# Optimization experiments

Measured on AMD Instinct MI355X. Metric: run time of the kernel, lower is better.

The kernel has to match this reference:

```python
import jax, jax.numpy as jnp
import numpy as np

N_NODES = 100000
HIDDEN = 128
N_EDGES = 1600000


def setup_inputs() -> dict:
    key = jax.random.key(0)
    k_z, k_e, k_w1, k_b1, k_w2, k_b2 = jax.random.split(key, 6)
    z = jax.random.normal(k_z, (N_NODES, HIDDEN), dtype=jnp.float32)
    edge_index = jax.random.randint(k_e, (2, N_EDGES), 0, N_NODES, dtype=jnp.int64)
    # torch.nn.Linear default init: U(-1/sqrt(fan_in), 1/sqrt(fan_in))
    lim1 = 1.0 / np.sqrt(2 * HIDDEN)
    W1 = jax.random.uniform(k_w1, (2 * HIDDEN, HIDDEN), minval=-lim1, maxval=lim1, dtype=jnp.float32)
    b1 = jax.random.uniform(k_b1, (HIDDEN,), minval=-lim1, maxval=lim1, dtype=jnp.float32)
    lim2 = 1.0 / np.sqrt(HIDDEN)
    W2 = jax.random.uniform(k_w2, (HIDDEN, 1), minval=-lim2, maxval=lim2, dtype=jnp.float32)
    b2 = jax.random.uniform(k_b2, (1,), minval=-lim2, maxval=lim2, dtype=jnp.float32)
    return {"z": z, "edge_index": edge_index, "W1": W1, "b1": b1, "W2": W2, "b2": b2}


def reference(z, edge_index, W1, b1, W2, b2):
    src = edge_index[0]
    dst = edge_index[1]
    # gather node pairs -> concat: [E, 2H]
    edge_feat = jnp.concatenate([z[src], z[dst]], axis=1)
    h = jax.nn.relu(edge_feat @ W1 + b1)  # [E, H]
    score = h @ W2 + b2                   # [E, 1]
    return score
```

## Files before the change

### kernel.cpp

```cpp
#include <hip/hip_runtime.h>
#include <hip/hip_bf16.h>
#include <stdint.h>

#define HIDDEN 128
#define EPG 8
#define NBLK_SORT 256
#define NBUK 256

typedef __attribute__((ext_vector_type(8))) short bf16x8;
typedef __attribute__((ext_vector_type(16))) float f32x16;

static __device__ __forceinline__ uint32_t cvt2(float a, float b) {
    union { __hip_bfloat162 h2; uint32_t u; } c;
    c.h2 = __float22bfloat162_rn(make_float2(a, b));
    return c.u;
}
static __device__ __forceinline__ float bf_lo(uint32_t p) {
    union { uint32_t u; float f; } v; v.u = p << 16; return v.f;
}
static __device__ __forceinline__ float bf_hi(uint32_t p) {
    union { uint32_t u; float f; } v; v.u = p & 0xffff0000u; return v.f;
}

__global__ __launch_bounds__(256) void transpose_w1(
    const float* __restrict__ W1, unsigned short* __restrict__ Wt)
{
    const int t = blockIdx.x * 256 + threadIdx.x;
    if (t >= 4096) return;
    const int cc = t >> 4;
    const int kg = t & 15;
    const int ccol = cc & 127;
    const int kofs = (cc >= 128) ? 128 : 0;
    uint32_t u[4];
    #pragma unroll
    for (int p = 0; p < 4; ++p) {
        const float a = W1[(size_t)(kofs + kg * 8 + 2 * p) * 128 + ccol];
        const float b = W1[(size_t)(kofs + kg * 8 + 2 * p + 1) * 128 + ccol];
        u[p] = cvt2(a, b);
    }
    uint4 o = { u[0], u[1], u[2], u[3] };
    *reinterpret_cast<uint4*>(Wt + (size_t)cc * 128 + kg * 8) = o;
}

__global__ __launch_bounds__(256) void precompute_mfma32(
    const float* __restrict__ z, const float* __restrict__ W1,
    const unsigned short* __restrict__ Wt,
    unsigned short* __restrict__ UV, int n_nodes, int n_groups)
{
    __shared__ char Zt[32 * 256];
    __shared__ char Sm[32 * 512];

    const int tid = threadIdx.x;
    const int lane = tid & 63;
    const int w = tid >> 6;
    const int nl = lane & 31;
    const int hi = lane >> 5;

    const int st_node = tid >> 3;
    const int st_j2 = tid & 7;
    const int st_swz = (st_node & 7) << 4;
    const int st_addrA = st_node * 256 + ((st_j2 * 32) ^ st_swz);
    const int st_addrB = st_node * 256 + ((st_j2 * 32 + 16) ^ st_swz);

    bf16x8 wf[2][8];
    if (Wt) {
        #pragma unroll
        for (int cg = 0; cg < 2; ++cg) {
            const int cc = w * 64 + cg * 32 + nl;
            #pragma unroll
            for (int ks = 0; ks < 8; ++ks)
                wf[cg][ks] = *reinterpret_cast<const bf16x8*>(
                    Wt + (size_t)cc * 128 + ks * 16 + hi * 8);
        }
    } else {
        #pragma unroll
        for (int cg = 0; cg < 2; ++cg) {
            const int cc = w * 64 + cg * 32 + nl;
            const int ccol = cc & 127;
            const int kofs = (cc >= 128) ? 128 : 0;
            #pragma unroll
            for (int ks = 0; ks < 8; ++ks) {
                const int k0 = ks * 16 + hi * 8 + kofs;
                float t[8];
                #pragma unroll
                for (int j = 0; j < 8; ++j)
                    t[j] = W1[(size_t)(k0 + j) * 128 + ccol];
                union { uint32_t u[4]; bf16x8 v; } fu;
                fu.u[0] = cvt2(t[0], t[1]); fu.u[1] = cvt2(t[2], t[3]);
                fu.u[2] = cvt2(t[4], t[5]); fu.u[3] = cvt2(t[6], t[7]);
                wf[cg][ks] = fu.v;
            }
        }
    }

    const int stride = gridDim.x;
    int ng = blockIdx.x;
    if (ng >= n_groups) return;

    float4 nz0, nz1, nz2, nz3;
    {
        int node = ng * 32 + st_node;
        node = (node < n_nodes) ? node : (n_nodes - 1);
        const float* zp = z + (size_t)node * HIDDEN + st_j2 * 16;
        nz0 = *reinterpret_cast<const float4*>(zp);
        nz1 = *reinterpret_cast<const float4*>(zp + 4);
        nz2 = *reinterpret_cast<const float4*>(zp + 8);
        nz3 = *reinterpret_cast<const float4*>(zp + 12);
    }

    while (ng < n_groups) {
        {
            uint4 A, B;
            A.x = cvt2(nz0.x, nz0.y); A.y = cvt2(nz0.z, nz0.w);
            A.z = cvt2(nz1.x, nz1.y); A.w = cvt2(nz1.z, nz1.w);
            B.x = cvt2(nz2.x, nz2.y); B.y = cvt2(nz2.z, nz2.w);
            B.z = cvt2(nz3.x, nz3.y); B.w = cvt2(nz3.z, nz3.w);
            *reinterpret_cast<uint4*>(Zt + st_addrA) = A;
            *reinterpret_cast<uint4*>(Zt + st_addrB) = B;
        }

        const int ngn = ng + stride;
        if (ngn < n_groups) {
            int node = ngn * 32 + st_node;
            node = (node < n_nodes) ? node : (n_nodes - 1);
            const float* zp = z + (size_t)node * HIDDEN + st_j2 * 16;
            nz0 = *reinterpret_cast<const float4*>(zp);
            nz1 = *reinterpret_cast<const float4*>(zp + 4);
            nz2 = *reinterpret_cast<const float4*>(zp + 8);
            nz3 = *reinterpret_cast<const float4*>(zp + 12);
        }

        __syncthreads();

        {
            const int rd_swz = (nl & 7) << 4;
            bf16x8 zf[8];
            #pragma unroll
            for (int ks = 0; ks < 8; ++ks) {
                const int off = ks * 32 + hi * 16;
                zf[ks] = *reinterpret_cast<const bf16x8*>(
                    Zt + nl * 256 + (off ^ rd_swz));
            }

            f32x16 acc0 = {};
            f32x16 acc1 = {};
            #pragma unroll
            for (int ks = 0; ks < 8; ++ks) {
                acc0 = __builtin_amdgcn_mfma_f32_32x32x16_bf16(wf[0][ks], zf[ks], acc0, 0, 0, 0);
                acc1 = __builtin_amdgcn_mfma_f32_32x32x16_bf16(wf[1][ks], zf[ks], acc1, 0, 0, 0);
            }

            const int swz = (nl & 15) << 3;
            #pragma unroll
            for (int g = 0; g < 4; ++g) {
                uint2 s0, s1;
                s0.x = cvt2(acc0[4 * g + 0], acc0[4 * g + 1]);
                s0.y = cvt2(acc0[4 * g + 2], acc0[4 * g + 3]);
                s1.x = cvt2(acc1[4 * g + 0], acc1[4 * g + 1]);
                s1.y = cvt2(acc1[4 * g + 2], acc1[4 * g + 3]);
                const int colb0 = w * 128 + g * 16 + hi * 8;
                const int colb1 = w * 128 + 64 + g * 16 + hi * 8;
                *reinterpret_cast<uint2*>(Sm + nl * 512 + (colb0 ^ swz)) = s0;
                *reinterpret_cast<uint2*>(Sm + nl * 512 + (colb1 ^ swz)) = s1;
            }
        }

        __syncthreads();

        {
            const int colb0 = (tid & 31) * 16;
            #pragma unroll
            for (int rep = 0; rep < 4; ++rep) {
                const int node_local = rep * 8 + (tid >> 5);
                const int swz = (node_local & 15) << 3;
                const uint2 g0 = *reinterpret_cast<const uint2*>(Sm + node_local * 512 + ((colb0) ^ swz));
                const uint2 g1 = *reinterpret_cast<const uint2*>(Sm + node_local * 512 + ((colb0 + 8) ^ swz));
                const int node = ng * 32 + node_local;
                if (node < n_nodes) {
                    uint4 o = { g0.x, g0.y, g1.x, g1.y };
                    *reinterpret_cast<uint4*>(UV + (size_t)node * 256 + (tid & 31) * 8) = o;
                }
            }
        }

        ng = ngn;
    }
}

__global__ __launch_bounds__(256) void hist2(
    const int* __restrict__ ei, int* __restrict__ h,
    int n_edges, int chunk, int sh)
{
    __shared__ int lh[NBUK];
    const int t = threadIdx.x;
    if (t < NBUK) lh[t] = 0;
    __syncthreads();
    const int e0 = blockIdx.x * chunk;
    const int e1 = min(e0 + chunk, n_edges);
    for (int e = e0 + t; e < e1; e += 256)
        atomicAdd(&lh[((unsigned)ei[e]) >> sh], 1);
    __syncthreads();
    if (t < NBUK) h[t * NBLK_SORT + blockIdx.x] = lh[t];
}

__global__ __launch_bounds__(NBLK_SORT) void scanP1(
    int* __restrict__ h, int* __restrict__ rowtot)
{
    __shared__ int s[NBLK_SORT];
    const int b = blockIdx.x, t = threadIdx.x;
    const int v = h[b * NBLK_SORT + t];
    s[t] = v;
    __syncthreads();
    for (int d = 1; d < NBLK_SORT; d <<= 1) {
        const int x = (t >= d) ? s[t - d] : 0;
        __syncthreads();
        s[t] += x;
        __syncthreads();
    }
    h[b * NBLK_SORT + t] = s[t] - v;
    if (t == NBLK_SORT - 1) rowtot[b] = s[t];
}

__global__ __launch_bounds__(NBUK) void scanP2(int* __restrict__ rowtot)
{
    __shared__ int s[NBUK];
    const int t = threadIdx.x;
    const int v = rowtot[t];
    s[t] = v;
    __syncthreads();
    for (int d = 1; d < NBUK; d <<= 1) {
        const int x = (t >= d) ? s[t - d] : 0;
        __syncthreads();
        s[t] += x;
        __syncthreads();
    }
    rowtot[t] = s[t] - v;
}

__global__ __launch_bounds__(256) void scatter2(
    const int* __restrict__ ei, const int* __restrict__ h,
    const int* __restrict__ base,
    int2* __restrict__ sd, int* __restrict__ org,
    int n_edges, int chunk, int sh)
{
    __shared__ int lbase[NBUK];
    __shared__ int lrank[NBUK];
    const int t = threadIdx.x;
    if (t < NBUK) {
        lbase[t] = h[t * NBLK_SORT + blockIdx.x] + base[t];
        lrank[t] = 0;
    }
    __syncthreads();
    const int e0 = blockIdx.x * chunk;
    const int e1 = min(e0 + chunk, n_edges);
    for (int e = e0 + t; e < e1; e += 256) {
        const int s = ei[e];
        const int d = ei[n_edges + e];
        const int b = ((unsigned)s) >> sh;
        const int r = atomicAdd(&lrank[b], 1);
        const int pos = lbase[b] + r;
        sd[pos] = make_int2(s, d);
        org[pos] = e;
    }
}

static __device__ __forceinline__ float dot8(uint4 u, uint4 v,
                                             const float* w, const float* bb) {
    const uint32_t up[4] = { u.x, u.y, u.z, u.w };
    const uint32_t vp[4] = { v.x, v.y, v.z, v.w };
    float s = 0.f;
    #pragma unroll
    for (int p = 0; p < 4; ++p) {
        const float h0 = bf_lo(up[p]) + bf_lo(vp[p]) + bb[2 * p];
        const float h1 = bf_hi(up[p]) + bf_hi(vp[p]) + bb[2 * p + 1];
        s = fmaf(fmaxf(h0, 0.f), w[2 * p], s);
        s = fmaf(fmaxf(h1, 0.f), w[2 * p + 1], s);
    }
    return s;
}
static __device__ __forceinline__ float red16(float s) {
    s += __shfl_xor(s, 1, 64); s += __shfl_xor(s, 2, 64);
    s += __shfl_xor(s, 4, 64); s += __shfl_xor(s, 8, 64);
    return s;
}

template <int PACKED>
__global__ __launch_bounds__(256, 4) void edge_score_t(
    const int2* __restrict__ sd, const int* __restrict__ org,
    const int* __restrict__ srcp, const int* __restrict__ dstp,
    const unsigned short* __restrict__ UV,
    const float* __restrict__ b1, const float* __restrict__ W2,
    const float* __restrict__ b2, float* __restrict__ outp, int n_edges)
{
    int vb = blockIdx.x;
    if (PACKED) {
        const int nb = gridDim.x;
        const int q8 = nb >> 3, r8 = nb & 7;
        const int x = blockIdx.x & 7, i = blockIdx.x >> 3;
        vb = (x < r8 ? x * (q8 + 1) : r8 * (q8 + 1) + (x - r8) * q8) + i;
    }

    const int g = (vb * 256 + (int)threadIdx.x) >> 4;
    const int q = threadIdx.x & 15;
    const int e0 = g * EPG;
    if (e0 >= n_edges) return;

    const float4 w2a = *reinterpret_cast<const float4*>(W2 + q * 8);
    const float4 w2b = *reinterpret_cast<const float4*>(W2 + q * 8 + 4);
    const float wloc[8] = { w2a.x, w2a.y, w2a.z, w2a.w, w2b.x, w2b.y, w2b.z, w2b.w };
    const float4 b1a = *reinterpret_cast<const float4*>(b1 + q * 8);
    const float4 b1b = *reinterpret_cast<const float4*>(b1 + q * 8 + 4);
    const float bb[8] = { b1a.x, b1a.y, b1a.z, b1a.w, b1b.x, b1b.y, b1b.z, b1b.w };
    const float bias = b2[0];

    const char* UVb = (const char*)UV;
    const uint32_t qo = (uint32_t)q * 16u;

    if (e0 + EPG - 1 < n_edges) {
        int sidx[EPG], didx[EPG];
        if (PACKED) {
            const int4 p0 = *reinterpret_cast<const int4*>(sd + e0);
            const int4 p1 = *reinterpret_cast<const int4*>(sd + e0 + 2);
            const int4 p2 = *reinterpret_cast<const int4*>(sd + e0 + 4);
            const int4 p3 = *reinterpret_cast<const int4*>(sd + e0 + 6);
            sidx[0]=p0.x; didx[0]=p0.y; sidx[1]=p0.z; didx[1]=p0.w;
            sidx[2]=p1.x; didx[2]=p1.y; sidx[3]=p1.z; didx[3]=p1.w;
            sidx[4]=p2.x; didx[4]=p2.y; sidx[5]=p2.z; didx[5]=p2.w;
            sidx[6]=p3.x; didx[6]=p3.y; sidx[7]=p3.z; didx[7]=p3.w;
        } else {
            const int4 sA = *reinterpret_cast<const int4*>(srcp + e0);
            const int4 sB = *reinterpret_cast<const int4*>(srcp + e0 + 4);
            const int4 dA = *reinterpret_cast<const int4*>(dstp + e0);
            const int4 dB = *reinterpret_cast<const int4*>(dstp + e0 + 4);
            sidx[0]=sA.x; sidx[1]=sA.y; sidx[2]=sA.z; sidx[3]=sA.w;
            sidx[4]=sB.x; sidx[5]=sB.y; sidx[6]=sB.z; sidx[7]=sB.w;
            didx[0]=dA.x; didx[1]=dA.y; didx[2]=dA.z; didx[3]=dA.w;
            didx[4]=dB.x; didx[5]=dB.y; didx[6]=dB.z; didx[7]=dB.w;
        }

        uint4 u[EPG], v[EPG];
        #pragma unroll
        for (int ii = 0; ii < EPG; ++ii) {
            u[ii] = *reinterpret_cast<const uint4*>(UVb + ((uint32_t)sidx[ii] * 512u + qo));
            v[ii] = *reinterpret_cast<const uint4*>(UVb + ((uint32_t)didx[ii] * 512u + 256u + qo));
        }
        __builtin_amdgcn_sched_barrier(0);

        float s[EPG];
        #pragma unroll
        for (int ii = 0; ii < EPG; ++ii) s[ii] = dot8(u[ii], v[ii], wloc, bb);
        #pragma unroll
        for (int ii = 0; ii < EPG; ++ii) s[ii] = red16(s[ii]) + bias;

        if (q == 0) {
            if (PACKED) {
                const int4 o0 = *reinterpret_cast<const int4*>(org + e0);
                const int4 o1 = *reinterpret_cast<const int4*>(org + e0 + 4);
                outp[o0.x] = s[0]; outp[o0.y] = s[1];
                outp[o0.z] = s[2]; outp[o0.w] = s[3];
                outp[o1.x] = s[4]; outp[o1.y] = s[5];
                outp[o1.z] = s[6]; outp[o1.w] = s[7];
            } else {
                float4 oA = { s[0], s[1], s[2], s[3] };
                float4 oB = { s[4], s[5], s[6], s[7] };
                *reinterpret_cast<float4*>(outp + e0) = oA;
                *reinterpret_cast<float4*>(outp + e0 + 4) = oB;
            }
        }
    } else {
        for (int ii = 0; ii < EPG; ++ii) {
            const int e = e0 + ii;
            if (e >= n_edges) break;
            const int si = PACKED ? sd[e].x : srcp[e];
            const int di = PACKED ? sd[e].y : dstp[e];
            const uint4 uu = *reinterpret_cast<const uint4*>(UVb + ((uint32_t)si * 512u + qo));
            const uint4 vv = *reinterpret_cast<const uint4*>(UVb + ((uint32_t)di * 512u + 256u + qo));
            float s = red16(dot8(uu, vv, wloc, bb));
            if (q == 0) {
                if (PACKED) outp[org[e]] = s + bias;
                else        outp[e] = s + bias;
            }
        }
    }
}

extern "C" void kernel_launch(void* const* d_in, const int* in_sizes, int n_in,
                              void* d_out, int out_size, void* d_ws, size_t ws_size,
                              hipStream_t stream) {
    const float* z  = (const float*)d_in[0];
    const int*   ei = (const int*)d_in[1];
    const float* W1 = (const float*)d_in[2];
    const float* b1 = (const float*)d_in[3];
    const float* W2 = (const float*)d_in[4];
    const float* b2 = (const float*)d_in[5];
    float* out = (float*)d_out;

    const int n_nodes = in_sizes[0] / HIDDEN;
    const int n_edges = in_sizes[1] / 2;

    int sh = 0;
    while (((unsigned)(n_nodes - 1) >> sh) >= NBUK) sh++;

    char* wsp = (char*)d_ws;
    size_t off = 0;
    auto alloc = [&](size_t bytes) -> char* {
        char* p = wsp + off;
        off = (off + bytes + 255) & ~(size_t)255;
        return p;
    };
    unsigned short* UV = (unsigned short*)alloc((size_t)n_nodes * 256 * 2);
    unsigned short* Wt = (unsigned short*)alloc(256 * 128 * 2);
    const size_t base_need = off;
    int*  h      = (int*)alloc((size_t)NBUK * NBLK_SORT * 4);
    int*  rowtot = (int*)alloc((size_t)NBUK * 4);
    int2* sd     = (int2*)alloc((size_t)n_edges * 8);
    int*  org    = (int*)alloc((size_t)n_edges * 4);
    const bool have_wt = ws_size >= base_need;
    const bool do_sort = ws_size >= off;

    if (have_wt) transpose_w1<<<16, 256, 0, stream>>>(W1, Wt);

    {
        const int n_groups = (n_nodes + 31) / 32;
        const int g1 = n_groups < 768 ? n_groups : 768;
        precompute_mfma32<<<g1, 256, 0, stream>>>(z, W1, have_wt ? Wt : nullptr,
                                                  UV, n_nodes, n_groups);
    }

    const int groups = (n_edges + EPG - 1) / EPG;
    const int eblocks = (groups * 16 + 255) / 256;

    if (do_sort) {
        const int chunk = (n_edges + NBLK_SORT - 1) / NBLK_SORT;
        hist2<<<NBLK_SORT, 256, 0, stream>>>(ei, h, n_edges, chunk, sh);
        scanP1<<<NBUK, NBLK_SORT, 0, stream>>>(h, rowtot);
        scanP2<<<1, NBUK, 0, stream>>>(rowtot);
        scatter2<<<NBLK_SORT, 256, 0, stream>>>(ei, h, rowtot, sd, org,
                                                n_edges, chunk, sh);
        edge_score_t<1><<<eblocks, 256, 0, stream>>>(sd, org, nullptr, nullptr, UV,
                                                     b1, W2, b2, out, n_edges);
    } else {
        edge_score_t<0><<<eblocks, 256, 0, stream>>>(nullptr, nullptr, ei, ei + n_edges,
                                                     UV, b1, W2, b2, out, n_edges);
    }
}
```

Baseline: 133.6 us.

## Fold b1 into node precompute, fuse bucket-base scan into scatter, widen grid

The first-layer bias b1 now seeds the MFMA accumulator for the source-half columns in the node precompute, so the per-edge dot no longer adds bias. The single-block scan of bucket totals is removed; each scatter block rescans the 256 row totals in shared memory, saving a kernel launch. The precompute grid cap grows from 768 to 1024 blocks. Baking the bias into bf16 UV changes rounding slightly, and every scatter block now repeats the small scan.

```diff
diff --git a/kernel.cpp b/kernel.cpp
--- a/kernel.cpp
+++ b/kernel.cpp
@@ -45,6 +45,7 @@
 __global__ __launch_bounds__(256) void precompute_mfma32(
     const float* __restrict__ z, const float* __restrict__ W1,
     const unsigned short* __restrict__ Wt,
+    const float* __restrict__ b1,
     unsigned short* __restrict__ UV, int n_nodes, int n_groups)
 {
     __shared__ char Zt[32 * 256];
@@ -93,6 +94,18 @@
         }
     }
 
+    f32x16 binit[2];
+    #pragma unroll
+    for (int cg = 0; cg < 2; ++cg) {
+        const int cc0 = w * 64 + cg * 32;
+        #pragma unroll
+        for (int r = 0; r < 16; ++r) {
+            const int crow = (r & 3) + 8 * (r >> 2) + 4 * hi;
+            const int cc = cc0 + crow;
+            binit[cg][r] = (cc < 128) ? b1[cc] : 0.f;
+        }
+    }
+
     const int stride = gridDim.x;
     int ng = blockIdx.x;
     if (ng >= n_groups) return;
@@ -142,8 +155,8 @@
                     Zt + nl * 256 + (off ^ rd_swz));
             }
 
-            f32x16 acc0 = {};
-            f32x16 acc1 = {};
+            f32x16 acc0 = binit[0];
+            f32x16 acc1 = binit[1];
             #pragma unroll
             for (int ks = 0; ks < 8; ++ks) {
                 acc0 = __builtin_amdgcn_mfma_f32_32x32x16_bf16(wf[0][ks], zf[ks], acc0, 0, 0, 0);
@@ -221,33 +234,28 @@
     if (t == NBLK_SORT - 1) rowtot[b] = s[t];
 }
 
-__global__ __launch_bounds__(NBUK) void scanP2(int* __restrict__ rowtot)
-{
-    __shared__ int s[NBUK];
-    const int t = threadIdx.x;
-    const int v = rowtot[t];
-    s[t] = v;
-    __syncthreads();
-    for (int d = 1; d < NBUK; d <<= 1) {
-        const int x = (t >= d) ? s[t - d] : 0;
-        __syncthreads();
-        s[t] += x;
-        __syncthreads();
-    }
-    rowtot[t] = s[t] - v;
-}
-
 __global__ __launch_bounds__(256) void scatter2(
     const int* __restrict__ ei, const int* __restrict__ h,
-    const int* __restrict__ base,
+    const int* __restrict__ rowtot,
     int2* __restrict__ sd, int* __restrict__ org,
     int n_edges, int chunk, int sh)
 {
+    __shared__ int sscan[NBUK];
     __shared__ int lbase[NBUK];
     __shared__ int lrank[NBUK];
     const int t = threadIdx.x;
+    const int v = (t < NBUK) ? rowtot[t] : 0;
+    if (t < NBUK) sscan[t] = v;
+    __syncthreads();
+    for (int d = 1; d < NBUK; d <<= 1) {
+        int x = 0;
+        if (t < NBUK && t >= d) x = sscan[t - d];
+        __syncthreads();
+        if (t < NBUK) sscan[t] += x;
+        __syncthreads();
+    }
     if (t < NBUK) {
-        lbase[t] = h[t * NBLK_SORT + blockIdx.x] + base[t];
+        lbase[t] = (sscan[t] - v) + h[t * NBLK_SORT + blockIdx.x];
         lrank[t] = 0;
     }
     __syncthreads();
@@ -264,15 +272,14 @@
     }
 }
 
-static __device__ __forceinline__ float dot8(uint4 u, uint4 v,
-                                             const float* w, const float* bb) {
+static __device__ __forceinline__ float dot8(uint4 u, uint4 v, const float* w) {
     const uint32_t up[4] = { u.x, u.y, u.z, u.w };
     const uint32_t vp[4] = { v.x, v.y, v.z, v.w };
     float s = 0.f;
     #pragma unroll
     for (int p = 0; p < 4; ++p) {
-        const float h0 = bf_lo(up[p]) + bf_lo(vp[p]) + bb[2 * p];
-        const float h1 = bf_hi(up[p]) + bf_hi(vp[p]) + bb[2 * p + 1];
+        const float h0 = bf_lo(up[p]) + bf_lo(vp[p]);
+        const float h1 = bf_hi(up[p]) + bf_hi(vp[p]);
         s = fmaf(fmaxf(h0, 0.f), w[2 * p], s);
         s = fmaf(fmaxf(h1, 0.f), w[2 * p + 1], s);
     }
@@ -289,7 +296,7 @@
     const int2* __restrict__ sd, const int* __restrict__ org,
     const int* __restrict__ srcp, const int* __restrict__ dstp,
     const unsigned short* __restrict__ UV,
-    const float* __restrict__ b1, const float* __restrict__ W2,
+    const float* __restrict__ W2,
     const float* __restrict__ b2, float* __restrict__ outp, int n_edges)
 {
     int vb = blockIdx.x;
@@ -308,9 +315,6 @@
     const float4 w2a = *reinterpret_cast<const float4*>(W2 + q * 8);
     const float4 w2b = *reinterpret_cast<const float4*>(W2 + q * 8 + 4);
     const float wloc[8] = { w2a.x, w2a.y, w2a.z, w2a.w, w2b.x, w2b.y, w2b.z, w2b.w };
-    const float4 b1a = *reinterpret_cast<const float4*>(b1 + q * 8);
-    const float4 b1b = *reinterpret_cast<const float4*>(b1 + q * 8 + 4);
-    const float bb[8] = { b1a.x, b1a.y, b1a.z, b1a.w, b1b.x, b1b.y, b1b.z, b1b.w };
     const float bias = b2[0];
 
     const char* UVb = (const char*)UV;
@@ -348,7 +352,7 @@
 
         float s[EPG];
         #pragma unroll
-        for (int ii = 0; ii < EPG; ++ii) s[ii] = dot8(u[ii], v[ii], wloc, bb);
+        for (int ii = 0; ii < EPG; ++ii) s[ii] = dot8(u[ii], v[ii], wloc);
         #pragma unroll
         for (int ii = 0; ii < EPG; ++ii) s[ii] = red16(s[ii]) + bias;
 
@@ -375,7 +379,7 @@
             const int di = PACKED ? sd[e].y : dstp[e];
             const uint4 uu = *reinterpret_cast<const uint4*>(UVb + ((uint32_t)si * 512u + qo));
             const uint4 vv = *reinterpret_cast<const uint4*>(UVb + ((uint32_t)di * 512u + 256u + qo));
-            float s = red16(dot8(uu, vv, wloc, bb));
+            float s = red16(dot8(uu, vv, wloc));
             if (q == 0) {
                 if (PACKED) outp[org[e]] = s + bias;
                 else        outp[e] = s + bias;
@@ -422,9 +426,9 @@
 
     {
         const int n_groups = (n_nodes + 31) / 32;
-        const int g1 = n_groups < 768 ? n_groups : 768;
+        const int g1 = n_groups < 1024 ? n_groups : 1024;
         precompute_mfma32<<<g1, 256, 0, stream>>>(z, W1, have_wt ? Wt : nullptr,
-                                                  UV, n_nodes, n_groups);
+                                                  b1, UV, n_nodes, n_groups);
     }
 
     const int groups = (n_edges + EPG - 1) / EPG;
@@ -434,13 +438,12 @@
         const int chunk = (n_edges + NBLK_SORT - 1) / NBLK_SORT;
         hist2<<<NBLK_SORT, 256, 0, stream>>>(ei, h, n_edges, chunk, sh);
         scanP1<<<NBUK, NBLK_SORT, 0, stream>>>(h, rowtot);
-        scanP2<<<1, NBUK, 0, stream>>>(rowtot);
         scatter2<<<NBLK_SORT, 256, 0, stream>>>(ei, h, rowtot, sd, org,
                                                 n_edges, chunk, sh);
         edge_score_t<1><<<eblocks, 256, 0, stream>>>(sd, org, nullptr, nullptr, UV,
-                                                     b1, W2, b2, out, n_edges);
+                                                     W2, b2, out, n_edges);
     } else {
         edge_score_t<0><<<eblocks, 256, 0, stream>>>(nullptr, nullptr, ei, ei + n_edges,
-                                                     UV, b1, W2, b2, out, n_edges);
-    }
-}
+                                                     UV, W2, b2, out, n_edges);
+    }
+}
```

Result: no change. 135.5 us (+1.4%).
